# Performance work log

Measured on AMD Instinct MI355X. Metric: run time of the kernel, lower is better.

## Reference

```python
import jax, jax.numpy as jnp
import numpy as np

HEADS = 8
SCALE_BASE = 512
EPS = 1e-5


def xpos(x, downscale=False):
    # x: (B, h, S, hd) ; XPOS rotary embedding with exponential scale
    hd = x.shape[-1]
    S = x.shape[-2]
    half = hd // 2
    base_scale = (jnp.arange(0, hd, 2, dtype=jnp.float32) + 0.4 * hd) / (1.4 * hd)  # (half,)
    pos = jnp.arange(S, dtype=jnp.float32)
    scale = base_scale[None, :] ** (pos[:, None] / SCALE_BASE)  # (S, half)
    inv_freq = 1.0 / (10000.0 ** (jnp.arange(half, dtype=jnp.float32) / half))
    sinu = pos[:, None] * inv_freq[None, :]  # (S, half)
    sin, cos = jnp.sin(sinu), jnp.cos(sinu)
    if downscale:
        scale = 1.0 / scale
    # duplicate_interleave: (S, half) -> (S, hd)
    sin_s = jnp.repeat(sin * scale, 2, axis=-1)
    cos_s = jnp.repeat(cos * scale, 2, axis=-1)
    x1 = x[..., ::2]
    x2 = x[..., 1::2]
    rot = jnp.stack((-x2, x1), axis=-1).reshape(x.shape)  # rotate_every_two
    return x * cos_s + rot * sin_s


def decay_mask(S):
    # (heads, S, S): gamma^(n-m) for n>=m else 0
    gammas = 1.0 - jnp.exp(jnp.linspace(np.log(1 / 32), np.log(1 / 512), HEADS)).astype(jnp.float32)
    n = jnp.arange(S, dtype=jnp.float32)
    diff = n[:, None] - n[None, :]
    lg = jnp.log(gammas)[:, None, None]
    return jnp.where(diff >= 0, jnp.exp(jnp.maximum(diff, 0.0) * lg), 0.0)


def layer_norm(x, w, b):
    mu = x.mean(-1, keepdims=True)
    var = x.var(-1, keepdims=True)
    return (x - mu) / jnp.sqrt(var + EPS) * w + b


def multiscale_retention(Xq, Xkv, Wq, Wk, Wv, Wg, Wo, gn_w, gn_b):
    # Xq: (B,S,d) query source; Xkv: (B,S,d) key/value source (== Xq for self)
    B, S, _ = Xq.shape
    Q = jnp.einsum('bsd,hde->bhse', Xq, Wq)
    K = jnp.einsum('btd,hde->bhte', Xkv, Wk)
    V = jnp.einsum('btd,hdv->bhtv', Xkv, Wv)
    Q = xpos(Q)
    K = xpos(K, downscale=True)
    D = decay_mask(S)  # (h,S,S)
    scores = jnp.einsum('bhse,bhte->bhst', Q, K) * D[None]
    Y = jnp.einsum('bhst,bhtv->bhsv', scores, V)  # (B,h,S,hv)
    h, hv = Y.shape[1], Y.shape[3]
    # GroupNorm(heads, v_dim) over each head's channels per token
    mu = Y.mean(-1, keepdims=True)
    var = Y.var(-1, keepdims=True)
    Yn = (Y - mu) / jnp.sqrt(var + EPS)
    Yn = Yn.transpose(0, 2, 1, 3).reshape(B, S, h * hv) * gn_w + gn_b
    gate = jax.nn.sigmoid(Xq @ Wg) * (Xq @ Wg)  # swish gate
    return (gate * Yn) @ Wo


def setup_inputs() -> dict:
    key = jax.random.key(0)
    ks = jax.random.split(key, 32)
    d, f, h, hd, hv, vd = 1024, 4096, 8, 128, 256, 2048
    B, S = 2, 2048
    inp = {
        'X': jax.random.normal(ks[0], (B, S, d), jnp.float32),
        'mem': jax.random.normal(ks[1], (B, S, d), jnp.float32),
        'ln1_w': jax.random.uniform(ks[2], (d,), jnp.float32, 0.5, 1.5),
        'ln1_b': jax.random.normal(ks[3], (d,), jnp.float32) * 0.1,
        'ln2_w': jax.random.uniform(ks[4], (d,), jnp.float32, 0.5, 1.5),
        'ln2_b': jax.random.normal(ks[5], (d,), jnp.float32) * 0.1,
        'Wq': jax.random.normal(ks[6], (h, d, hd), jnp.float32) / d,
        'Wk': jax.random.normal(ks[7], (h, d, hd), jnp.float32) / d,
        'Wv': jax.random.normal(ks[8], (h, d, hv), jnp.float32) / d,
        'Wg': jax.random.normal(ks[9], (d, vd), jnp.float32) / d,
        'Wo': jax.random.normal(ks[10], (vd, d), jnp.float32) / d,
        'gn_w': jax.random.uniform(ks[11], (vd,), jnp.float32, 0.5, 1.5),
        'gn_b': jax.random.normal(ks[12], (vd,), jnp.float32) * 0.1,
        'cWq': jax.random.normal(ks[13], (h, d, hd), jnp.float32) / d,
        'cWk': jax.random.normal(ks[14], (h, d, hd), jnp.float32) / d,
        'cWv': jax.random.normal(ks[15], (h, d, hv), jnp.float32) / d,
        'cWg': jax.random.normal(ks[16], (d, vd), jnp.float32) / d,
        'cWo': jax.random.normal(ks[17], (vd, d), jnp.float32) / d,
        'cgn_w': jax.random.uniform(ks[18], (vd,), jnp.float32, 0.5, 1.5),
        'cgn_b': jax.random.normal(ks[19], (vd,), jnp.float32) * 0.1,
        'W1': jax.random.normal(ks[20], (d, f), jnp.float32) * (1.0 / np.sqrt(d)),
        'b1': jax.random.normal(ks[21], (f,), jnp.float32) * 0.02,
        'W2': jax.random.normal(ks[22], (f, d), jnp.float32) * (1.0 / np.sqrt(f)),
        'b2': jax.random.normal(ks[23], (d,), jnp.float32) * 0.02,
    }
    return inp


def reference(X, mem, ln1_w, ln1_b, ln2_w, ln2_b, Wq, Wk, Wv, Wg, Wo, gn_w, gn_b,
              cWq, cWk, cWv, cWg, cWo, cgn_w, cgn_b, W1, b1, W2, b2):
    # self retention block
    X = multiscale_retention(layer_norm(X, ln1_w, ln1_b), None, Wq, Wk, Wv, Wg, Wo, gn_w, gn_b) + X if False else multiscale_retention(layer_norm(X, ln1_w, ln1_b), layer_norm(X, ln1_w, ln1_b), Wq, Wk, Wv, Wg, Wo, gn_w, gn_b) + X
    # cross retention block (note: original reuses layer_norms_2 for both this and the FFN)
    h2 = layer_norm(X, ln2_w, ln2_b)
    X = multiscale_retention(h2, mem, cWq, cWk, cWv, cWg, cWo, cgn_w, cgn_b) + X
    # FFN block (GELU exact, per torch nn.GELU default)
    h3 = layer_norm(X, ln2_w, ln2_b)
    X = (jax.nn.gelu(h3 @ W1 + b1, approximate=False) @ W2 + b2) + X
    return X
```

## Files before the change

### kernel.cpp

```cpp
#include <hip/hip_runtime.h>
#include <math.h>

#define RTOT 4096
#define SEQQ 2048

typedef unsigned int uint32;
typedef __attribute__((ext_vector_type(4))) float f32x4;
typedef __attribute__((ext_vector_type(8))) short bf16x8;

__device__ __forceinline__ unsigned short f2bf(float f) {
  unsigned int u = __float_as_uint(f);
  u = (u + 0x7FFFu + ((u >> 16) & 1u)) >> 16;
  return (unsigned short)u;
}
__device__ __forceinline__ float bf2f(unsigned short h) {
  return __uint_as_float(((unsigned int)h) << 16);
}
__device__ __forceinline__ void gld16(const void* g, void* l) {
  __builtin_amdgcn_global_load_lds(
      (const __attribute__((address_space(1))) uint32*)g,
      (__attribute__((address_space(3))) uint32*)l, 16, 0, 0);
}
__device__ __forceinline__ void bar() {
  asm volatile("" ::: "memory");
  __builtin_amdgcn_s_barrier();
  asm volatile("" ::: "memory");
}
#define VMCNT(n) asm volatile("s_waitcnt vmcnt(" #n ")" ::: "memory")

__device__ __forceinline__ void tr_tile(
    const float* __restrict__ in, unsigned short* __restrict__ out,
    int R, int C, int perm, int bx, int by, int z) {
  __shared__ float t[32][33];
  in  += (size_t)z * R * C;
  out += (size_t)z * C * R;
  int r0 = bx * 32, c0 = by * 32;
  int tx = threadIdx.x & 31, ty = threadIdx.x >> 5;
  #pragma unroll
  for (int i = 0; i < 4; ++i) {
    int r = ty + i * 8;
    t[r][tx] = in[(size_t)(r0 + r) * C + c0 + tx];
  }
  __syncthreads();
  #pragma unroll
  for (int i = 0; i < 4; ++i) {
    int cc = c0 + ty + i * 8;
    if (perm) cc = 64 * (cc >> 6) + ((cc & 1) << 5) + ((cc & 63) >> 1);
    out[(size_t)cc * R + r0 + tx] = f2bf(t[tx][ty + i * 8]);
  }
}

__device__ __forceinline__ void tab_body(float* __restrict__ tab, int blk) {
  int i = blk * 256 + threadIdx.x;
  int pos = i >> 6, j = i & 63;
  float bs = (2.f * (float)j + 51.2f) * (1.f / 179.2f);
  float e = (float)pos * (1.f / 512.f);
  float sc = exp2f(e * log2f(bs));
  float invf = exp2f(-(float)j * (13.287712379549449f / 64.f));
  float su, cu;
  sincosf((float)pos * invf, &su, &cu);
  tab[i]            = cu * sc;
  tab[131072 + i]   = su * sc;
  float si = 1.f / sc;
  tab[262144 + i]   = cu * si;
  tab[393216 + i]   = su * si;
}

__device__ __forceinline__ void ln_row(const float* __restrict__ x,
    const float* __restrict__ w, const float* __restrict__ b,
    unsigned short* __restrict__ out, int row) {
  __shared__ float red[2][4];
  int tid = threadIdx.x;
  const float* xr = x + (size_t)row * 1024;
  float4 v = *(const float4*)(xr + tid * 4);
  float s  = v.x + v.y + v.z + v.w;
  float ss = v.x*v.x + v.y*v.y + v.z*v.z + v.w*v.w;
  #pragma unroll
  for (int o = 32; o > 0; o >>= 1) { s += __shfl_down(s, o); ss += __shfl_down(ss, o); }
  int wid = tid >> 6;
  if ((tid & 63) == 0) { red[0][wid] = s; red[1][wid] = ss; }
  __syncthreads();
  float st  = red[0][0] + red[0][1] + red[0][2] + red[0][3];
  float sst = red[1][0] + red[1][1] + red[1][2] + red[1][3];
  float mu   = st * (1.f / 1024.f);
  float var  = sst * (1.f / 1024.f) - mu * mu;
  float rstd = rsqrtf(var + 1e-5f);
  float4 wv = *(const float4*)(w + tid * 4);
  float4 bv = *(const float4*)(b + tid * 4);
  unsigned short o0 = f2bf((v.x - mu) * rstd * wv.x + bv.x);
  unsigned short o1 = f2bf((v.y - mu) * rstd * wv.y + bv.y);
  unsigned short o2 = f2bf((v.z - mu) * rstd * wv.z + bv.z);
  unsigned short o3 = f2bf((v.w - mu) * rstd * wv.w + bv.w);
  ushort4 o4 = make_ushort4(o0, o1, o2, o3);
  *(ushort4*)(out + (size_t)row * 1024 + tid * 4) = o4;
}

__device__ __forceinline__ void cvt_body(const float* __restrict__ in,
    unsigned short* __restrict__ out, int blk) {
  int i = blk * 256 + threadIdx.x;
  const float4* p = (const float4*)(in + (size_t)i * 8);
  float4 a = p[0], b = p[1];
  bf16x8 v;
  v[0] = (short)f2bf(a.x); v[1] = (short)f2bf(a.y); v[2] = (short)f2bf(a.z); v[3] = (short)f2bf(a.w);
  v[4] = (short)f2bf(b.x); v[5] = (short)f2bf(b.y); v[6] = (short)f2bf(b.z); v[7] = (short)f2bf(b.w);
  *(bf16x8*)(out + (size_t)i * 8) = v;
}

__global__ __launch_bounds__(256) void prep1(
    const float* Wq, const float* Wk, const float* Wg, const float* Wv,
    const float* Wo, unsigned short* WqkgT, unsigned short* WvT,
    unsigned short* WoT, float* tab,
    const float* X, const float* ln1w, const float* ln1b, unsigned short* hbuf) {
  int idx = blockIdx.x;
  if (idx < 1024)      { tr_tile(Wq, WqkgT,               1024, 128, 1, idx & 31, (idx >> 5) & 3, idx >> 7); }
  else if (idx < 2048) { int i = idx - 1024; tr_tile(Wk, WqkgT + 1024 * 1024, 1024, 128, 1, i & 31, (i >> 5) & 3, i >> 7); }
  else if (idx < 4096) { int i = idx - 2048; tr_tile(Wg, WqkgT + 2048 * 1024, 1024, 2048, 0, i & 31, i >> 5, 0); }
  else if (idx < 6144) { int i = idx - 4096; tr_tile(Wv, WvT, 1024, 256, 0, i & 31, (i >> 5) & 7, i >> 8); }
  else if (idx < 8192) { int i = idx - 6144; tr_tile(Wo, WoT, 2048, 1024, 0, i & 63, i >> 6, 0); }
  else if (idx < 8704) { tab_body(tab, idx - 8192); }
  else                 { ln_row(X, ln1w, ln1b, hbuf, idx - 8704); }
}

__global__ __launch_bounds__(256) void prep2(
    const float* cWq, const float* cWg, const float* cWk, const float* cWv,
    const float* cWo, unsigned short* cQGT, unsigned short* cWkT,
    unsigned short* cWvT, unsigned short* cWoT,
    const float* mem, unsigned short* mem16,
    const float* out, const float* ln2w, const float* ln2b, unsigned short* hbuf) {
  int idx = blockIdx.x;
  if (idx < 1024)       { tr_tile(cWq, cQGT,               1024, 128, 1, idx & 31, (idx >> 5) & 3, idx >> 7); }
  else if (idx < 3072)  { int i = idx - 1024; tr_tile(cWg, cQGT + 1024 * 1024, 1024, 2048, 0, i & 31, i >> 5, 0); }
  else if (idx < 4096)  { int i = idx - 3072; tr_tile(cWk, cWkT, 1024, 128, 1, i & 31, (i >> 5) & 3, i >> 7); }
  else if (idx < 6144)  { int i = idx - 4096; tr_tile(cWv, cWvT, 1024, 256, 0, i & 31, (i >> 5) & 7, i >> 8); }
  else if (idx < 8192)  { int i = idx - 6144; tr_tile(cWo, cWoT, 2048, 1024, 0, i & 63, i >> 6, 0); }
  else if (idx < 10240) { cvt_body(mem, mem16, idx - 8192); }
  else                  { ln_row(out, ln2w, ln2b, hbuf, idx - 10240); }
}

__global__ __launch_bounds__(256) void prep3(
    const float* W1, const float* W2, unsigned short* W1T, unsigned short* W2T,
    const float* out, const float* ln2w, const float* ln2b, unsigned short* hbuf) {
  int idx = blockIdx.x;
  if (idx < 4096)      { tr_tile(W1, W1T, 1024, 4096, 0, idx & 31, idx >> 5, 0); }
  else if (idx < 8192) { int i = idx - 4096; tr_tile(W2, W2T, 4096, 1024, 0, i & 127, i >> 7, 0); }
  else                 { ln_row(out, ln2w, ln2b, hbuf, idx - 8192); }
}

enum { EPI_F32_RES = 0, EPI_BF16 = 1, EPI_XPOS = 2, EPI_GELU = 4, EPI_BRES = 5,
       EPI_QKG = 6, EPI_QG = 7 };

struct EpiP {
  void* C; int ldc;
  const float* bias; const float* resid;
  const float* tab;
  unsigned short* oQ; unsigned short* oK; unsigned short* oG;
};

template<int EPI>
__device__ __forceinline__ void epi_store(size_t m, int n, int N0, float v, const EpiP& P) {
  if constexpr (EPI == EPI_BF16) {
    ((unsigned short*)P.C)[m * P.ldc + n] = f2bf(v);
  } else if constexpr (EPI == EPI_GELU) {
    v += P.bias[n];
    v = 0.5f * v * (1.f + erff(v * 0.70710678f));
    ((unsigned short*)P.C)[m * P.ldc + n] = f2bf(v);
  } else if constexpr (EPI == EPI_BRES) {
    v += P.bias[n] + P.resid[m * P.ldc + n];
    ((float*)P.C)[m * P.ldc + n] = v;
  } else {
    v += P.resid[m * P.ldc + n];
    ((float*)P.C)[m * P.ldc + n] = v;
  }
}

template<int EPI>
__global__ __launch_bounds__(256) void gemm_mfma(
    const unsigned short* __restrict__ A, int lda,
    const unsigned short* __restrict__ Bt, int ldb, int K, int nbx, EpiP P) {
  __shared__ __align__(16) unsigned short As[2][2][128 * 32];
  __shared__ __align__(16) unsigned short Bs[2][2][128 * 32];
  const int tid = threadIdx.x, w = tid >> 6, lane = tid & 63;
  int q8 = (int)gridDim.x >> 3;
  int sbid = ((int)blockIdx.x & 7) * q8 + ((int)blockIdx.x >> 3);
  int by = sbid / nbx, bx = sbid - by * nbx;
  const int M0 = by * 128, N0 = bx * 128;
  const int fr = lane & 15, fs = lane >> 4;
  const int srow = lane >> 2, sp = lane & 3;

  f32x4 zf = {0.f, 0.f, 0.f, 0.f};
  f32x4 acc[4][4];
  #pragma unroll
  for (int i = 0; i < 4; ++i)
    #pragma unroll
    for (int j = 0; j < 4; ++j) acc[i][j] = zf;

  auto STAGE = [&](int buf, int k0) {
    #pragma unroll
    for (int kk = 0; kk < 2; ++kk)
      #pragma unroll
      for (int c = 0; c < 4; ++c) {
        int ch = w * 4 + c;
        int cc = ch & 7;
        int row = cc * 16 + srow;
        int so = sp ^ ((row >> 1) & 3);
        if (ch < 8) gld16(A  + (size_t)(M0 + row) * lda + k0 + kk * 32 + so * 8, &As[buf][kk][cc * 512]);
        else        gld16(Bt + (size_t)(N0 + row) * ldb + k0 + kk * 32 + so * 8, &Bs[buf][kk][cc * 512]);
      }
  };

  const int NT = K >> 6;
  STAGE(0, 0);
  int cur = 0;
  for (int t = 0; t < NT; ++t) {
    if (t + 1 < NT) { STAGE(cur ^ 1, (t + 1) * 64); VMCNT(8); }
    else            { VMCNT(0); }
    bar();
    #pragma unroll
    for (int kk = 0; kk < 2; ++kk) {
      bf16x8 af[4], bfr[4];
      #pragma unroll
      for (int mi = 0; mi < 4; ++mi) {
        int row = (w >> 1) * 64 + mi * 16 + fr;
        af[mi] = *(const bf16x8*)(&As[cur][kk][row * 32 + (fs ^ ((row >> 1) & 3)) * 8]);
      }
      #pragma unroll
      for (int ni = 0; ni < 4; ++ni) {
        int row = (w & 1) * 64 + ni * 16 + fr;
        bfr[ni] = *(const bf16x8*)(&Bs[cur][kk][row * 32 + (fs ^ ((row >> 1) & 3)) * 8]);
      }
      #pragma unroll
      for (int mi = 0; mi < 4; ++mi)
        #pragma unroll
        for (int ni = 0; ni < 4; ++ni)
          acc[mi][ni] = __builtin_amdgcn_mfma_f32_16x16x32_bf16(af[mi], bfr[ni], acc[mi][ni], 0, 0, 0);
    }
    bar();
    cur ^= 1;
  }

  #pragma unroll
  for (int mi = 0; mi < 4; ++mi)
    #pragma unroll
    for (int r = 0; r < 4; ++r) {
      size_t m = M0 + (w >> 1) * 64 + mi * 16 + fs * 4 + r;
      #pragma unroll
      for (int ni = 0; ni < 4; ++ni) {
        int n = N0 + (w & 1) * 64 + ni * 16 + fr;
        epi_store<EPI>(m, n, N0, acc[mi][ni][r], P);
      }
    }
}

template<int EPI>
__global__ __launch_bounds__(256) void gemm_bn64(
    const unsigned short* __restrict__ A, int lda,
    const unsigned short* __restrict__ Bt, int ldb, int K, int nbx, EpiP P) {
  __shared__ __align__(16) unsigned short As[2][2][128 * 32];
  __shared__ __align__(16) unsigned short Bs[2][2][64 * 32];
  const int tid = threadIdx.x, w = tid >> 6, lane = tid & 63;
  int q8 = (int)gridDim.x >> 3;
  int sbid = ((int)blockIdx.x & 7) * q8 + ((int)blockIdx.x >> 3);
  int by = sbid / nbx, bx = sbid - by * nbx;
  const int M0 = by * 128, N0 = bx * 64;
  const int fr = lane & 15, fs = lane >> 4;
  const int srow = lane >> 2, sp = lane & 3;

  f32x4 zf = {0.f, 0.f, 0.f, 0.f};
  f32x4 acc[2][4];
  #pragma unroll
  for (int i = 0; i < 2; ++i)
    #pragma unroll
    for (int j = 0; j < 4; ++j) acc[i][j] = zf;

  auto STAGE = [&](int buf, int k0) {
    #pragma unroll
    for (int kk = 0; kk < 2; ++kk)
      #pragma unroll
      for (int c = 0; c < 3; ++c) {
        int ch = w * 3 + c;
        if (ch < 8) {
          int row = ch * 16 + srow;
          int so = sp ^ ((row >> 1) & 3);
          gld16(A + (size_t)(M0 + row) * lda + k0 + kk * 32 + so * 8, &As[buf][kk][ch * 512]);
        } else {
          int bch = ch - 8;
          int row = bch * 16 + srow;
          int so = sp ^ ((row >> 1) & 3);
          gld16(Bt + (size_t)(N0 + row) * ldb + k0 + kk * 32 + so * 8, &Bs[buf][kk][bch * 512]);
        }
      }
  };

  const int NT = K >> 6;
  STAGE(0, 0);
  int cur = 0;
  for (int t = 0; t < NT; ++t) {
    if (t + 1 < NT) { STAGE(cur ^ 1, (t + 1) * 64); VMCNT(6); }
    else            { VMCNT(0); }
    bar();
    #pragma unroll
    for (int kk = 0; kk < 2; ++kk) {
      bf16x8 af[2], bfr[4];
      #pragma unroll
      for (int mi = 0; mi < 2; ++mi) {
        int row = w * 32 + mi * 16 + fr;
        af[mi] = *(const bf16x8*)(&As[cur][kk][row * 32 + (fs ^ ((row >> 1) & 3)) * 8]);
      }
      #pragma unroll
      for (int ni = 0; ni < 4; ++ni) {
        int row = ni * 16 + fr;
        bfr[ni] = *(const bf16x8*)(&Bs[cur][kk][row * 32 + (fs ^ ((row >> 1) & 3)) * 8]);
      }
      #pragma unroll
      for (int mi = 0; mi < 2; ++mi)
        #pragma unroll
        for (int ni = 0; ni < 4; ++ni)
          acc[mi][ni] = __builtin_amdgcn_mfma_f32_16x16x32_bf16(af[mi], bfr[ni], acc[mi][ni], 0, 0, 0);
    }
    bar();
    cur ^= 1;
  }

  if constexpr (EPI == EPI_XPOS) {
    int gsel = (N0 >> 6) & 1;
    #pragma unroll
    for (int mi = 0; mi < 2; ++mi)
      #pragma unroll
      for (int r = 0; r < 4; ++r) {
        size_t m = M0 + w * 32 + mi * 16 + fs * 4 + r;
        int pos = (int)(m & (SEQQ - 1));
        #pragma unroll
        for (int ni = 0; ni < 2; ++ni) {
          int j = gsel * 32 + ni * 16 + fr;
          float cs = P.tab[pos * 64 + j], sn = P.tab[131072 + pos * 64 + j];
          float ve = acc[mi][ni][r], vo = acc[mi][ni + 2][r];
          unsigned short* dst = (unsigned short*)P.C;
          dst[m * P.ldc + N0 + ni * 16 + fr]       = f2bf(ve * cs - vo * sn);
          dst[m * P.ldc + N0 + (ni + 2) * 16 + fr] = f2bf(vo * cs + ve * sn);
        }
      }
  } else {
    #pragma unroll
    for (int mi = 0; mi < 2; ++mi)
      #pragma unroll
      for (int r = 0; r < 4; ++r) {
        size_t m = M0 + w * 32 + mi * 16 + fs * 4 + r;
        #pragma unroll
        for (int ni = 0; ni < 4; ++ni) {
          int n = N0 + ni * 16 + fr;
          epi_store<EPI>(m, n, N0, acc[mi][ni][r], P);
        }
      }
  }
}

template<int EPI>
__global__ __launch_bounds__(512, 2) void gemm256(
    const unsigned short* __restrict__ A,
    const unsigned short* __restrict__ Bt,
    int nbx, EpiP P) {
  __shared__ __align__(16) unsigned short lds[4][2][8192];
  const int tid = threadIdx.x, w = tid >> 6, lane = tid & 63;
  int cpx = (int)gridDim.x >> 3;
  int sbid = ((int)blockIdx.x & 7) * cpx + ((int)blockIdx.x >> 3);
  int by = sbid / nbx, bx = sbid - by * nbx;
  const int M0 = by * 256, N0 = bx * 256;
  const int wm = w >> 2, wn = w & 3;
  const int fr = lane & 15, fs = lane >> 4;
  const int srow = lane >> 2;
  const int sslot = (lane & 3) ^ ((lane >> 3) & 3);
  const int rsw = (fr >> 1) & 3;

  f32x4 acc[8][4];
  #pragma unroll
  for (int i = 0; i < 8; ++i)
    #pragma unroll
    for (int j = 0; j < 4; ++j) acc[i][j] = {0.f, 0.f, 0.f, 0.f};

  auto STAGE = [&](int t, int buf) {
    int k0 = t * 32;
    #pragma unroll
    for (int j = 0; j < 4; ++j) {
      int c = w * 4 + j;
      if (c < 16)
        gld16(A  + (size_t)(M0 + c * 16 + srow) * 1024 + k0 + sslot * 8,
              &lds[buf][0][c * 512]);
      else
        gld16(Bt + (size_t)(N0 + (c - 16) * 16 + srow) * 1024 + k0 + sslot * 8,
              &lds[buf][1][(c - 16) * 512]);
    }
  };
  auto COMPUTE = [&](int t) {
    const unsigned short* la = &lds[t & 3][0][wm * 128 * 32];
    const unsigned short* lb = &lds[t & 3][1][wn * 64 * 32];
    bf16x8 a[8], b[4];
    #pragma unroll
    for (int ni = 0; ni < 4; ++ni)
      b[ni] = *(const bf16x8*)(lb + (ni * 16 + fr) * 32 + ((fs ^ rsw) * 8));
    #pragma unroll
    for (int mi = 0; mi < 8; ++mi)
      a[mi] = *(const bf16x8*)(la + (mi * 16 + fr) * 32 + ((fs ^ rsw) * 8));
    #pragma unroll
    for (int mi = 0; mi < 8; ++mi)
      #pragma unroll
      for (int ni = 0; ni < 4; ++ni)
        acc[mi][ni] = __builtin_amdgcn_mfma_f32_16x16x32_bf16(a[mi], b[ni], acc[mi][ni], 0, 0, 0);
  };

  STAGE(0, 0); STAGE(1, 1); STAGE(2, 2);
  for (int t = 0; t < 29; ++t) {
    STAGE(t + 3, (t + 3) & 3);
    VMCNT(12);
    bar();
    COMPUTE(t);
    bar();
  }
  VMCNT(8);  bar(); COMPUTE(29); bar();
  VMCNT(4);  bar(); COMPUTE(30); bar();
  VMCNT(0);  bar(); COMPUTE(31);

  if constexpr (EPI == EPI_GELU) {
    #pragma unroll
    for (int mi = 0; mi < 8; ++mi)
      #pragma unroll
      for (int r = 0; r < 4; ++r) {
        size_t m = M0 + wm * 128 + mi * 16 + fs * 4 + r;
        #pragma unroll
        for (int ni = 0; ni < 4; ++ni) {
          int n = N0 + wn * 64 + ni * 16 + fr;
          float v = acc[mi][ni][r] + P.bias[n];
          v = 0.5f * v * (1.f + erff(v * 0.70710678f));
          ((unsigned short*)P.C)[m * P.ldc + n] = f2bf(v);
        }
      }
  } else {
    const int nb = N0 + wn * 64;
    const bool isQ = nb < 1024;
    const bool isK = (EPI == EPI_QKG) && !isQ && (nb < 2048);
    if (isQ || isK) {
      const float* tc = isK ? P.tab + 262144 : P.tab;
      const float* ts = tc + 131072;
      unsigned short* dst = isK ? P.oK : P.oQ;
      const int nloc = isK ? nb - 1024 : nb;
      const int gsel = (nloc >> 6) & 1;
      #pragma unroll
      for (int mi = 0; mi < 8; ++mi)
        #pragma unroll
        for (int r = 0; r < 4; ++r) {
          size_t m = M0 + wm * 128 + mi * 16 + fs * 4 + r;
          int pos = (int)(m & (SEQQ - 1));
          #pragma unroll
          for (int ni = 0; ni < 2; ++ni) {
            int j = gsel * 32 + ni * 16 + fr;
            float cs = tc[pos * 64 + j], sn = ts[pos * 64 + j];
            float ve = acc[mi][ni][r], vo = acc[mi][ni + 2][r];
            dst[m * 1024 + nloc + ni * 16 + fr]       = f2bf(ve * cs - vo * sn);
            dst[m * 1024 + nloc + (ni + 2) * 16 + fr] = f2bf(vo * cs + ve * sn);
          }
        }
    } else {
      const int nloc = nb - ((EPI == EPI_QKG) ? 2048 : 1024);
      #pragma unroll
      for (int mi = 0; mi < 8; ++mi)
        #pragma unroll
        for (int r = 0; r < 4; ++r) {
          size_t m = M0 + wm * 128 + mi * 16 + fs * 4 + r;
          #pragma unroll
          for (int ni = 0; ni < 4; ++ni) {
            float v = acc[mi][ni][r];
            P.oG[m * 2048 + nloc + ni * 16 + fr] = f2bf(v / (1.f + expf(-v)));
          }
        }
    }
  }
}

__global__ __launch_bounds__(256) void retention_part(
    const unsigned short* __restrict__ Qx, const unsigned short* __restrict__ Kx,
    const unsigned short* __restrict__ VT,
    unsigned short* __restrict__ Y0, unsigned short* __restrict__ Y1) {
  __shared__ __align__(16) unsigned short Ks[2][32 * 128];
  __shared__ __align__(16) unsigned short Vs[2][256 * 32];
  const int tid = threadIdx.x, w = tid >> 6, lane = tid & 63;
  int bid = blockIdx.x;
  int th = bid >> 9;
  int rr = bid & 511;
  int qt, h, b;
  if (rr < 256) { qt = 31 - (rr >> 3); h = rr & 7; b = 0; }
  else          { int k = rr - 256; qt = k >> 3; h = k & 7; b = 1; }
  const int q0 = qt * 64;
  const int fr = lane & 15, fs = lane >> 4;

  float gamma = 1.f - expf(-3.4657359028f - 0.3960841032f * (float)h);
  float l2g = log2f(gamma);
  const int qglob = q0 + w * 16 + fr;

  size_t qrow = (size_t)b * SEQQ + qglob;
  bf16x8 qf[4];
  #pragma unroll
  for (int ks = 0; ks < 4; ++ks)
    qf[ks] = *(const bf16x8*)(Qx + qrow * 1024 + h * 128 + ks * 32 + fs * 8);

  float gtl8[8];
  #pragma unroll
  for (int i = 0; i < 8; ++i) {
    int toff = (i >> 2) * 16 + fs * 4 + (i & 3);
    gtl8[i] = exp2f(-(float)toff * l2g);
  }

  f32x4 zf = {0.f, 0.f, 0.f, 0.f};
  f32x4 yacc[16];
  #pragma unroll
  for (int i = 0; i < 16; ++i) yacc[i] = zf;

  int cutoff = (int)(16.f / (-l2g));
  int t_start = q0 - cutoff;
  if (t_start < 0) t_start = 0;
  t_start &= ~31;
  size_t kbase = (size_t)b * SEQQ;

  auto STAGE = [&](int buf, int t0) {
    #pragma unroll
    for (int c = 0; c < 2; ++c) {
      int ch = w * 2 + c;
      int row = ch * 4 + (lane >> 4);
      int so = (lane & 15) ^ (row & 15);
      gld16(Kx + (kbase + t0 + row) * 1024 + h * 128 + so * 8, &Ks[buf][ch * 512]);
    }
    #pragma unroll
    for (int c = 0; c < 4; ++c) {
      int ch = w * 4 + c;
      int vrow = ch * 16 + (lane >> 2);
      int so = (lane & 3) ^ ((vrow >> 1) & 3);
      gld16(VT + (size_t)(h * 256 + vrow) * RTOT + kbase + t0 + so * 8, &Vs[buf][ch * 512]);
    }
  };

  const int nt_total = (q0 + 64 - t_start) >> 5;
  const int n0 = (nt_total + 1) >> 1;
  const int it0 = th ? n0 : 0;
  const int it1 = th ? nt_total : n0;
  unsigned short* Yp = th ? Y1 : Y0;

  STAGE(0, t_start + it0 * 32);
  int cur = 0;
  for (int it = it0; it < it1; ++it) {
    int t0 = t_start + it * 32;
    if (it + 1 < it1) { STAGE(cur ^ 1, t0 + 32); VMCNT(6); }
    else              { VMCNT(0); }
    bar();

    f32x4 sacc[2];
    sacc[0] = zf; sacc[1] = zf;
    #pragma unroll
    for (int nt = 0; nt < 2; ++nt) {
      int row = nt * 16 + fr;
      #pragma unroll
      for (int ks = 0; ks < 4; ++ks) {
        int sl = ks * 4 + fs;
        bf16x8 kf = *(const bf16x8*)(&Ks[cur][row * 128 + (sl ^ (row & 15)) * 8]);
        sacc[nt] = __builtin_amdgcn_mfma_f32_16x16x32_bf16(kf, qf[ks], sacc[nt], 0, 0, 0);
      }
    }
    float fsc = exp2f((float)(qglob - t0) * l2g);
    uint32 pk[4];
    #pragma unroll
    for (int nt = 0; nt < 2; ++nt)
      #pragma unroll
      for (int hf = 0; hf < 2; ++hf) {
        int r0i = hf * 2;
        int ta = t0 + nt * 16 + fs * 4 + r0i;
        float va = (qglob >= ta)     ? sacc[nt][r0i]     * (fsc * gtl8[nt * 4 + r0i])     : 0.f;
        float vb = (qglob >= ta + 1) ? sacc[nt][r0i + 1] * (fsc * gtl8[nt * 4 + r0i + 1]) : 0.f;
        pk[nt * 2 + hf] = (uint32)f2bf(va) | ((uint32)f2bf(vb) << 16);
      }
    union { uint32 u[4]; bf16x8 v8; } pa;
    #pragma unroll
    for (int j = 0; j < 4; ++j) {
      int src = fr + 16 * (2 * (fs & 1) + (j >> 1));
      int v0 = __shfl((int)pk[j & 1],     src);
      int v1 = __shfl((int)pk[2 + (j & 1)], src);
      pa.u[j] = (fs < 2) ? (uint32)v0 : (uint32)v1;
    }
    #pragma unroll
    for (int nv = 0; nv < 16; ++nv) {
      int vrow = nv * 16 + fr;
      bf16x8 vf = *(const bf16x8*)(&Vs[cur][vrow * 32 + (fs ^ ((vrow >> 1) & 3)) * 8]);
      yacc[nv] = __builtin_amdgcn_mfma_f32_16x16x32_bf16(pa.v8, vf, yacc[nv], 0, 0, 0);
    }
    bar();
    cur ^= 1;
  }

  #pragma unroll
  for (int r = 0; r < 4; ++r) {
    int srow = q0 + w * 16 + fs * 4 + r;
    size_t mrow = (size_t)b * SEQQ + srow;
    unsigned short* orow = Yp + mrow * 2048 + h * 256;
    #pragma unroll
    for (int nv = 0; nv < 16; ++nv)
      orow[nv * 16 + fr] = f2bf(yacc[nv][r]);
  }
}

__global__ __launch_bounds__(256) void combine_gn(
    const unsigned short* __restrict__ Y0, const unsigned short* __restrict__ Y1,
    const unsigned short* __restrict__ Gate,
    const float* __restrict__ gnw, const float* __restrict__ gnb,
    unsigned short* __restrict__ Gout) {
  int idx = blockIdx.x * 4 + (threadIdx.x >> 6);
  int lane = threadIdx.x & 63;
  int h = idx & 7;
  size_t row = (size_t)(idx >> 3);
  size_t base = row * 2048 + h * 256 + lane * 4;
  ushort4 a = *(const ushort4*)(Y0 + base);
  ushort4 bb = *(const ushort4*)(Y1 + base);
  float y0 = bf2f(a.x) + bf2f(bb.x);
  float y1 = bf2f(a.y) + bf2f(bb.y);
  float y2 = bf2f(a.z) + bf2f(bb.z);
  float y3 = bf2f(a.w) + bf2f(bb.w);
  float s  = y0 + y1 + y2 + y3;
  float sq = y0*y0 + y1*y1 + y2*y2 + y3*y3;
  #pragma unroll
  for (int o = 32; o > 0; o >>= 1) { s += __shfl_xor(s, o); sq += __shfl_xor(sq, o); }
  float mu = s * (1.f / 256.f);
  float var = sq * (1.f / 256.f) - mu * mu;
  float rstd = rsqrtf(var + 1e-5f);
  int gi = h * 256 + lane * 4;
  float4 w4 = *(const float4*)(gnw + gi);
  float4 b4 = *(const float4*)(gnb + gi);
  ushort4 g4 = *(const ushort4*)(Gate + base);
  ushort4 o4;
  o4.x = f2bf(bf2f(g4.x) * ((y0 - mu) * rstd * w4.x + b4.x));
  o4.y = f2bf(bf2f(g4.y) * ((y1 - mu) * rstd * w4.y + b4.y));
  o4.z = f2bf(bf2f(g4.z) * ((y2 - mu) * rstd * w4.z + b4.z));
  o4.w = f2bf(bf2f(g4.w) * ((y3 - mu) * rstd * w4.w + b4.w));
  *(ushort4*)(Gout + base) = o4;
}

extern "C" void kernel_launch(void* const* d_in, const int* in_sizes, int n_in,
                              void* d_out, int out_size, void* d_ws, size_t ws_size,
                              hipStream_t stream) {
  const float* X    = (const float*)d_in[0];
  const float* mem  = (const float*)d_in[1];
  const float* ln1w = (const float*)d_in[2];
  const float* ln1b = (const float*)d_in[3];
  const float* ln2w = (const float*)d_in[4];
  const float* ln2b = (const float*)d_in[5];
  const float* Wq   = (const float*)d_in[6];
  const float* Wk   = (const float*)d_in[7];
  const float* Wv   = (const float*)d_in[8];
  const float* Wg   = (const float*)d_in[9];
  const float* Wo   = (const float*)d_in[10];
  const float* gnw  = (const float*)d_in[11];
  const float* gnb  = (const float*)d_in[12];
  const float* cWq  = (const float*)d_in[13];
  const float* cWk  = (const float*)d_in[14];
  const float* cWv  = (const float*)d_in[15];
  const float* cWg  = (const float*)d_in[16];
  const float* cWo  = (const float*)d_in[17];
  const float* cgnw = (const float*)d_in[18];
  const float* cgnb = (const float*)d_in[19];
  const float* W1   = (const float*)d_in[20];
  const float* b1   = (const float*)d_in[21];
  const float* W2   = (const float*)d_in[22];
  const float* b2   = (const float*)d_in[23];
  float* out = (float*)d_out;

  const size_t MB = 1024ull * 1024ull;
  if (ws_size < 106 * MB) return;
  unsigned char* W8 = (unsigned char*)d_ws;
  unsigned short* WqkgT = (unsigned short*)(W8 + 0 * MB);
  unsigned short* WvT   = (unsigned short*)(W8 + 8 * MB);
  unsigned short* WoT   = (unsigned short*)(W8 + 12 * MB);
  unsigned short* cQGT  = (unsigned short*)(W8 + 16 * MB);
  unsigned short* cWkT  = (unsigned short*)(W8 + 22 * MB);
  unsigned short* cWvT  = (unsigned short*)(W8 + 24 * MB);
  unsigned short* cWoT  = (unsigned short*)(W8 + 28 * MB);
  float*          tab   = (float*)(W8 + 32 * MB);
  unsigned short* hbuf  = (unsigned short*)(W8 + 34 * MB);
  unsigned short* Qx    = (unsigned short*)(W8 + 42 * MB);
  unsigned short* Kx    = (unsigned short*)(W8 + 50 * MB);
  unsigned short* W1T   = Qx;
  unsigned short* W2T   = Kx;
  unsigned short* VTb   = (unsigned short*)(W8 + 58 * MB);
  unsigned short* Gg    = (unsigned short*)(W8 + 74 * MB);
  unsigned short* Tb    = VTb;
  unsigned short* GoutB = (unsigned short*)(W8 + 90 * MB);
  unsigned short* mem16 = GoutB;
  unsigned short* Yp1a  = (unsigned short*)(W8 + 16 * MB);
  unsigned short* Yp1b  = (unsigned short*)(W8 + 0 * MB);

  EpiP P{};

  prep1<<<12800, 256, 0, stream>>>(Wq, Wk, Wg, Wv, Wo, WqkgT, WvT, WoT, tab,
                                   X, ln1w, ln1b, hbuf);

  P = EpiP{nullptr, 0, nullptr, nullptr, tab, Qx, Kx, Gg};
  gemm256<EPI_QKG><<<256, 512, 0, stream>>>(hbuf, WqkgT, 16, P);
  P = EpiP{VTb, 4096, nullptr, nullptr, nullptr, nullptr, nullptr, nullptr};
  gemm_mfma<EPI_BF16><<<512, 256, 0, stream>>>(WvT, 1024, hbuf, 1024, 1024, 32, P);
  retention_part<<<dim3(1024), 256, 0, stream>>>(Qx, Kx, VTb, GoutB, Yp1a);
  combine_gn<<<RTOT * 2, 256, 0, stream>>>(GoutB, Yp1a, Gg, gnw, gnb, GoutB);
  P = EpiP{out, 1024, nullptr, X, nullptr, nullptr, nullptr, nullptr};
  gemm_bn64<EPI_F32_RES><<<512, 256, 0, stream>>>(GoutB, 2048, WoT, 2048, 2048, 16, P);

  prep2<<<14336, 256, 0, stream>>>(cWq, cWg, cWk, cWv, cWo, cQGT, cWkT, cWvT, cWoT,
                                   mem, mem16, out, ln2w, ln2b, hbuf);

  P = EpiP{nullptr, 0, nullptr, nullptr, tab, Qx, nullptr, Gg};
  gemm256<EPI_QG><<<192, 512, 0, stream>>>(hbuf, cQGT, 12, P);
  P = EpiP{Kx, 1024, nullptr, nullptr, tab + 262144, nullptr, nullptr, nullptr};
  gemm_bn64<EPI_XPOS><<<512, 256, 0, stream>>>(mem16, 1024, cWkT, 1024, 1024, 16, P);
  P = EpiP{VTb, 4096, nullptr, nullptr, nullptr, nullptr, nullptr, nullptr};
  gemm_mfma<EPI_BF16><<<512, 256, 0, stream>>>(cWvT, 1024, mem16, 1024, 1024, 32, P);
  retention_part<<<dim3(1024), 256, 0, stream>>>(Qx, Kx, VTb, GoutB, Yp1b);
  combine_gn<<<RTOT * 2, 256, 0, stream>>>(GoutB, Yp1b, Gg, cgnw, cgnb, GoutB);
  P = EpiP{out, 1024, nullptr, out, nullptr, nullptr, nullptr, nullptr};
  gemm_bn64<EPI_F32_RES><<<512, 256, 0, stream>>>(GoutB, 2048, cWoT, 2048, 2048, 16, P);

  prep3<<<12288, 256, 0, stream>>>(W1, W2, W1T, W2T, out, ln2w, ln2b, hbuf);

  P = EpiP{Tb, 4096, b1, nullptr, nullptr, nullptr, nullptr, nullptr};
  gemm256<EPI_GELU><<<256, 512, 0, stream>>>(hbuf, W1T, 16, P);
  P = EpiP{out, 1024, b2, out, nullptr, nullptr, nullptr, nullptr};
  gemm_bn64<EPI_BRES><<<512, 256, 0, stream>>>(Tb, 4096, W2T, 4096, 4096, 16, P);
}
```

Before: 529.8 us.

## Restructure gemm256 pipeline to double-buffered 64-wide K stages

Replaces the 4-deep pipeline of 32-wide K tiles with a 2-deep double buffer of 64-wide K tiles, computing two 32-wide sub-tiles per barrier pair. This halves the number of barrier pairs and loop iterations, cutting synchronisation overhead. In exchange, prefetch distance drops from three tiles ahead to one, so less global-load latency can be hidden behind compute. The LDS footprint stays the same.

```diff
diff --git a/kernel.cpp b/kernel.cpp
--- a/kernel.cpp
+++ b/kernel.cpp
@@ -359,7 +359,7 @@
     const unsigned short* __restrict__ A,
     const unsigned short* __restrict__ Bt,
     int nbx, EpiP P) {
-  __shared__ __align__(16) unsigned short lds[4][2][8192];
+  __shared__ __align__(16) unsigned short lds[2][2][2][8192];
   const int tid = threadIdx.x, w = tid >> 6, lane = tid & 63;
   int cpx = (int)gridDim.x >> 3;
   int sbid = ((int)blockIdx.x & 7) * cpx + ((int)blockIdx.x >> 3);
@@ -378,21 +378,23 @@
     for (int j = 0; j < 4; ++j) acc[i][j] = {0.f, 0.f, 0.f, 0.f};
 
   auto STAGE = [&](int t, int buf) {
-    int k0 = t * 32;
-    #pragma unroll
-    for (int j = 0; j < 4; ++j) {
-      int c = w * 4 + j;
-      if (c < 16)
-        gld16(A  + (size_t)(M0 + c * 16 + srow) * 1024 + k0 + sslot * 8,
-              &lds[buf][0][c * 512]);
-      else
-        gld16(Bt + (size_t)(N0 + (c - 16) * 16 + srow) * 1024 + k0 + sslot * 8,
-              &lds[buf][1][(c - 16) * 512]);
-    }
+    int k0 = t * 64;
+    #pragma unroll
+    for (int kk = 0; kk < 2; ++kk)
+      #pragma unroll
+      for (int j = 0; j < 4; ++j) {
+        int c = w * 4 + j;
+        if (c < 16)
+          gld16(A  + (size_t)(M0 + c * 16 + srow) * 1024 + k0 + kk * 32 + sslot * 8,
+                &lds[buf][kk][0][c * 512]);
+        else
+          gld16(Bt + (size_t)(N0 + (c - 16) * 16 + srow) * 1024 + k0 + kk * 32 + sslot * 8,
+                &lds[buf][kk][1][(c - 16) * 512]);
+      }
   };
-  auto COMPUTE = [&](int t) {
-    const unsigned short* la = &lds[t & 3][0][wm * 128 * 32];
-    const unsigned short* lb = &lds[t & 3][1][wn * 64 * 32];
+  auto COMPUTE = [&](int buf, int kk) {
+    const unsigned short* la = &lds[buf][kk][0][wm * 128 * 32];
+    const unsigned short* lb = &lds[buf][kk][1][wn * 64 * 32];
     bf16x8 a[8], b[4];
     #pragma unroll
     for (int ni = 0; ni < 4; ++ni)
@@ -407,17 +409,18 @@
         acc[mi][ni] = __builtin_amdgcn_mfma_f32_16x16x32_bf16(a[mi], b[ni], acc[mi][ni], 0, 0, 0);
   };
 
-  STAGE(0, 0); STAGE(1, 1); STAGE(2, 2);
-  for (int t = 0; t < 29; ++t) {
-    STAGE(t + 3, (t + 3) & 3);
-    VMCNT(12);
+  const int NT = 16;
+  STAGE(0, 0);
+  int cur = 0;
+  for (int t = 0; t < NT; ++t) {
+    if (t + 1 < NT) { STAGE(t + 1, cur ^ 1); VMCNT(8); }
+    else            { VMCNT(0); }
     bar();
-    COMPUTE(t);
+    COMPUTE(cur, 0);
+    COMPUTE(cur, 1);
     bar();
-  }
-  VMCNT(8);  bar(); COMPUTE(29); bar();
-  VMCNT(4);  bar(); COMPUTE(30); bar();
-  VMCNT(0);  bar(); COMPUTE(31);
+    cur ^= 1;
+  }
 
   if constexpr (EPI == EPI_GELU) {
     #pragma unroll
```

New measurement: 532.6 us. No clear change (+0.5%).
